# Performance work log

Hardware: AMD Instinct MI355X
Metric: run time of the kernel (lower is better)

The kernel has to match this reference:

```python
import jax, jax.numpy as jnp
import numpy as np


def setup_inputs() -> dict:
    key = jax.random.key(0)
    k1, k2, k3, k4, k5 = jax.random.split(key, 5)
    B, T, C = 64, 1024, 768
    scale = 1.0 / np.sqrt(C)
    tokens = jax.random.normal(k1, (B, T, C), dtype=jnp.float32)
    mask_topk = jax.random.randint(k2, (B, T), 0, 2) > 0
    Wq = jax.random.normal(k3, (C, C), dtype=jnp.float32) * scale
    Wk = jax.random.normal(k4, (C, C), dtype=jnp.float32) * scale
    Wv = jax.random.normal(k5, (C, C), dtype=jnp.float32) * scale
    return {"tokens": tokens, "mask_topk": mask_topk, "Wq": Wq, "Wk": Wk, "Wv": Wv}


def reference(tokens, mask_topk, Wq, Wk, Wv):
    # tokens: [B, T, C]; mask_topk: [B, T] bool; W*: [C, C] (torch Linear weight, y = x @ W.T)
    C = tokens.shape[-1]
    m = mask_topk.astype(tokens.dtype)                      # [B, T]
    cnt = jnp.sum(m, axis=-1, keepdims=True)                # [B, 1]
    masked_sum = jnp.einsum('btc,bt->bc', tokens, m)        # [B, C]
    mean_all = jnp.mean(tokens, axis=1)                     # fallback when mask is empty
    q_sal = jnp.where(cnt > 0, masked_sum / jnp.maximum(cnt, 1.0), mean_all)  # [B, C]
    q_sal = q_sal[:, None, :]                               # [B, 1, C]

    Q = jnp.einsum('bqc,dc->bqd', q_sal, Wq)                # [B, 1, C]
    K = jnp.einsum('btc,dc->btd', tokens, Wk)               # [B, T, C]
    V = jnp.einsum('btc,dc->btd', tokens, Wv)               # [B, T, C]

    scores = jnp.einsum('bqd,btd->bqt', Q, K) / jnp.sqrt(jnp.asarray(C, tokens.dtype))
    attn = jax.nn.softmax(scores, axis=-1)                  # [B, 1, T]
    v_fg = jnp.einsum('bqt,btd->bqd', attn, V)[:, 0, :]     # [B, C]
    return (v_fg, attn)
```

## Files before the change

kernel.cpp:

```cpp
#include <hip/hip_runtime.h>
#include <hip/hip_bf16.h>

#define B 64
#define T 1024
#define C 768
#define TSPLIT 32
#define TCHUNK (T / TSPLIT)

#define OFF_MSUM   64
#define OFF_ASUM   (OFF_MSUM + B*TSPLIT*C)
#define OFF_CNT    (OFF_ASUM + B*TSPLIT*C)
#define OFF_Q      (OFF_CNT + B*TSPLIT)
#define OFF_QK     (OFF_Q + B*C)
#define OFF_SCORES (OFF_QK + B*C)
#define OFF_MPART  (OFF_SCORES + B*T)
#define OFF_SPART  (OFF_MPART + B*TSPLIT)
#define OFF_PPART  (OFF_SPART + B*TSPLIT)

__device__ __forceinline__ bool read_mask(const void* mask, int mode, int idx) {
    if (mode == 1) return ((const unsigned char*)mask)[idx] != 0;
    if (mode == 2) return ((const float*)mask)[idx] != 0.0f;
    return ((const int*)mask)[idx] != 0;
}

__global__ void k_detect(const void* mask, int* mode_out) {
    __shared__ int s_not01, s_isf;
    int tid = threadIdx.x;
    if (tid == 0) { s_not01 = 0; s_isf = 0; }
    __syncthreads();
    const int* mi = (const int*)mask;
    int not01 = 0, isf = 0;
    for (int k = 0; k < 64; ++k) {
        int v = mi[tid + 256 * k];
        if (v != 0 && v != 1) not01 = 1;
        if (v == 0x3F800000) isf = 1;
    }
    if (not01) atomicOr(&s_not01, 1);
    if (isf)   atomicOr(&s_isf, 1);
    __syncthreads();
    if (tid == 0) *mode_out = s_isf ? 2 : (s_not01 ? 1 : 0);
}

__global__ __launch_bounds__(192) void
k_pass1(const float* __restrict__ tokens, const void* mask, const int* modep,
        float* __restrict__ msum, float* __restrict__ asum, float* __restrict__ cntpart) {
    int ts = blockIdx.x, b = blockIdx.y, tid = threadIdx.x;
    int mode = *modep;
    __shared__ float s_m[TCHUNK];
    if (tid < TCHUNK)
        s_m[tid] = read_mask(mask, mode, b * T + ts * TCHUNK + tid) ? 1.f : 0.f;
    __syncthreads();
    int c = tid * 4;
    float4 ms = {0, 0, 0, 0}, as = {0, 0, 0, 0};
    const float* tb = tokens + (size_t)b * T * C;
#pragma unroll 4
    for (int r = 0; r < TCHUNK; ++r) {
        int t = ts * TCHUNK + r;
        float4 x = *(const float4*)(tb + (size_t)t * C + c);
        as.x += x.x; as.y += x.y; as.z += x.z; as.w += x.w;
        float wm = s_m[r];
        ms.x += wm * x.x; ms.y += wm * x.y; ms.z += wm * x.z; ms.w += wm * x.w;
    }
    size_t o = (size_t)(b * TSPLIT + ts) * C + c;
    *(float4*)(msum + o) = ms;
    *(float4*)(asum + o) = as;
    if (tid == 0) {
        float cnt = 0.f;
#pragma unroll
        for (int r = 0; r < TCHUNK; ++r) cnt += s_m[r];
        cntpart[b * TSPLIT + ts] = cnt;
    }
}

__global__ __launch_bounds__(256) void
k_qsal_rowdot(const float* __restrict__ msum, const float* __restrict__ asum,
              const float* __restrict__ cntpart, const float* __restrict__ Wq,
              float* __restrict__ Qv) {
    int b = blockIdx.y, tid = threadIdx.x;
    __shared__ float sq[C];
    float cnt = 0.f;
#pragma unroll
    for (int p = 0; p < TSPLIT; ++p) cnt += cntpart[b * TSPLIT + p];
    bool um = (cnt > 0.f);
    float scale = um ? (1.f / fmaxf(cnt, 1.f)) : (1.f / (float)T);
    const float* src = um ? msum : asum;
    for (int c = tid; c < C; c += 256) {
        float a = 0.f;
#pragma unroll 8
        for (int p = 0; p < TSPLIT; ++p) a += src[(size_t)(b * TSPLIT + p) * C + c];
        sq[c] = a * scale;
    }
    __syncthreads();
    int d = blockIdx.x * 64 + (tid >> 2), sub = tid & 3;
    const float4* w = (const float4*)(Wq + (size_t)d * C);
    const float4* v4 = (const float4*)sq;
    float acc = 0.f;
#pragma unroll 8
    for (int j = sub * 48; j < sub * 48 + 48; ++j) {
        float4 a = v4[j], x = w[j];
        acc += a.x * x.x + a.y * x.y + a.z * x.z + a.w * x.w;
    }
    acc += __shfl_xor(acc, 1);
    acc += __shfl_xor(acc, 2);
    if (sub == 0) Qv[b * C + d] = acc;
}

__global__ __launch_bounds__(256) void
k_coldot(const float* __restrict__ Qv, const float* __restrict__ Wk,
         float* __restrict__ qk) {
    int b = blockIdx.y, tid = threadIdx.x;
    __shared__ float sQ[C];
    for (int c = tid; c < C; c += 256) sQ[c] = Qv[b * C + c];
    __syncthreads();
    int c = blockIdx.x * 64 + (tid >> 2), sub = tid & 3;
    float acc = 0.f;
#pragma unroll 8
    for (int i = 0; i < 192; ++i) {
        int d = sub * 192 + i;
        acc += sQ[d] * Wk[(size_t)d * C + c];
    }
    acc += __shfl_xor(acc, 1);
    acc += __shfl_xor(acc, 2);
    if (sub == 0) qk[b * C + c] = acc * 0.03608439182435161f;
}

__global__ __launch_bounds__(192) void
k_fused(const float* __restrict__ tokens, const float* __restrict__ qk,
        float* __restrict__ scores, float* __restrict__ mpart,
        float* __restrict__ spart, float* __restrict__ ppart) {
    __shared__ float sq[C];
    __shared__ float ssc[TCHUNK];
    __shared__ float sw[TCHUNK];
    int ts = blockIdx.x, b = blockIdx.y, tid = threadIdx.x;
    ((float4*)sq)[tid] = ((const float4*)(qk + (size_t)b * C))[tid];
    __syncthreads();
    int wave = tid >> 6, lane = tid & 63;
    const float* tb = tokens + (size_t)b * T * C;
    const float4* q4 = (const float4*)sq;
    for (int r = wave; r < TCHUNK; r += 3) {
        int t = ts * TCHUNK + r;
        const float4* row = (const float4*)(tb + (size_t)t * C);
        float acc = 0.f;
#pragma unroll
        for (int j = 0; j < 3; ++j) {
            int idx = lane + 64 * j;
            float4 x = row[idx], q = q4[idx];
            acc += x.x * q.x + x.y * q.y + x.z * q.z + x.w * q.w;
        }
        for (int s = 32; s > 0; s >>= 1) acc += __shfl_xor(acc, s);
        if (lane == 0) { ssc[r] = acc; scores[(size_t)b * T + t] = acc; }
    }
    __syncthreads();
    float m = -3.4e38f;
#pragma unroll
    for (int r = 0; r < TCHUNK; ++r) m = fmaxf(m, ssc[r]);
    if (tid < TCHUNK) sw[tid] = expf(ssc[tid] - m);
    __syncthreads();
    float s = 0.f;
#pragma unroll
    for (int r = 0; r < TCHUNK; ++r) s += sw[r];
    int c = tid * 4;
    float4 acc = {0, 0, 0, 0};
#pragma unroll 4
    for (int r = 0; r < TCHUNK; ++r) {
        int t = ts * TCHUNK + r;
        float wv = sw[r];
        float4 x = *(const float4*)(tb + (size_t)t * C + c);
        acc.x += wv * x.x; acc.y += wv * x.y; acc.z += wv * x.z; acc.w += wv * x.w;
    }
    *(float4*)(ppart + (size_t)(b * TSPLIT + ts) * C + c) = acc;
    if (tid == 0) { mpart[b * TSPLIT + ts] = m; spart[b * TSPLIT + ts] = s; }
}

__global__ __launch_bounds__(256) void
k_attn(const float* __restrict__ scores, const float* __restrict__ mpart,
       const float* __restrict__ spart, float* __restrict__ attn) {
    int b = blockIdx.x, tid = threadIdx.x;
    float M = -3.4e38f;
#pragma unroll
    for (int p = 0; p < TSPLIT; ++p) M = fmaxf(M, mpart[b * TSPLIT + p]);
    float Z = 0.f;
#pragma unroll
    for (int p = 0; p < TSPLIT; ++p) Z += spart[b * TSPLIT + p] * expf(mpart[b * TSPLIT + p] - M);
    float invZ = 1.f / Z;
    float4 sc = ((const float4*)(scores + (size_t)b * T))[tid];
    float4 o;
    o.x = expf(sc.x - M) * invZ; o.y = expf(sc.y - M) * invZ;
    o.z = expf(sc.z - M) * invZ; o.w = expf(sc.w - M) * invZ;
    ((float4*)(attn + (size_t)b * T))[tid] = o;
}

__global__ __launch_bounds__(256) void
k_vfg(const float* __restrict__ ppart, const float* __restrict__ mpart,
      const float* __restrict__ spart, const float* __restrict__ Wv,
      float* __restrict__ vfg) {
    int b = blockIdx.y, tid = threadIdx.x;
    __shared__ float sp[C];
    float M = -3.4e38f;
#pragma unroll
    for (int p = 0; p < TSPLIT; ++p) M = fmaxf(M, mpart[b * TSPLIT + p]);
    float Z = 0.f;
#pragma unroll
    for (int p = 0; p < TSPLIT; ++p) Z += spart[b * TSPLIT + p] * expf(mpart[b * TSPLIT + p] - M);
    float invZ = 1.f / Z;
    float coef[TSPLIT];
#pragma unroll
    for (int p = 0; p < TSPLIT; ++p) coef[p] = expf(mpart[b * TSPLIT + p] - M) * invZ;
    for (int c = tid; c < C; c += 256) {
        float a = 0.f;
#pragma unroll 8
        for (int p = 0; p < TSPLIT; ++p)
            a += coef[p] * ppart[(size_t)(b * TSPLIT + p) * C + c];
        sp[c] = a;
    }
    __syncthreads();
    int d = blockIdx.x * 64 + (tid >> 2), sub = tid & 3;
    const float4* w = (const float4*)(Wv + (size_t)d * C);
    const float4* v4 = (const float4*)sp;
    float acc = 0.f;
#pragma unroll 8
    for (int j = sub * 48; j < sub * 48 + 48; ++j) {
        float4 a = v4[j], x = w[j];
        acc += a.x * x.x + a.y * x.y + a.z * x.z + a.w * x.w;
    }
    acc += __shfl_xor(acc, 1);
    acc += __shfl_xor(acc, 2);
    if (sub == 0) vfg[b * C + d] = acc;
}

extern "C" void kernel_launch(void* const* d_in, const int* in_sizes, int n_in,
                              void* d_out, int out_size, void* d_ws, size_t ws_size,
                              hipStream_t stream) {
    const float* tokens = (const float*)d_in[0];
    const void*  mask   = d_in[1];
    const float* Wq     = (const float*)d_in[2];
    const float* Wk     = (const float*)d_in[3];
    const float* Wv     = (const float*)d_in[4];

    float* ws      = (float*)d_ws;
    int*   mode    = (int*)d_ws;
    float* msum    = ws + OFF_MSUM;
    float* asum    = ws + OFF_ASUM;
    float* cntpart = ws + OFF_CNT;
    float* Qv      = ws + OFF_Q;
    float* qk      = ws + OFF_QK;
    float* scores  = ws + OFF_SCORES;
    float* mpart   = ws + OFF_MPART;
    float* spart   = ws + OFF_SPART;
    float* ppart   = ws + OFF_PPART;

    float* v_fg = (float*)d_out;
    float* attn = (float*)d_out + B * C;

    k_detect<<<1, 256, 0, stream>>>(mask, mode);
    k_pass1<<<dim3(TSPLIT, B), 192, 0, stream>>>(tokens, mask, mode, msum, asum, cntpart);
    k_qsal_rowdot<<<dim3(12, B), 256, 0, stream>>>(msum, asum, cntpart, Wq, Qv);
    k_coldot<<<dim3(12, B), 256, 0, stream>>>(Qv, Wk, qk);
    k_fused<<<dim3(TSPLIT, B), 192, 0, stream>>>(tokens, qk, scores, mpart, spart, ppart);
    k_attn<<<B, 256, 0, stream>>>(scores, mpart, spart, attn);
    k_vfg<<<dim3(12, B), 256, 0, stream>>>(ppart, mpart, spart, Wv, v_fg);
}
```

Baseline: 172.4 us.

## Batch four rows per block in weight matvecs to reuse weight loads

Splits the pooling/reduction steps out of the Wq and Wv matvec kernels into separate kernels, then makes each matvec block handle four batch rows at once so each weight element loaded is reused four times. The Wk column-dot kernel is batched the same way. The aim is to cut redundant weight traffic, since the whole 768x768 weight matrix was previously reread once per batch. The cost is an extra kernel launch, an extra round trip of the pooled vectors through global memory, and fewer blocks (192 instead of 768) for the matvecs.

```diff
diff --git a/kernel.cpp b/kernel.cpp
--- a/kernel.cpp
+++ b/kernel.cpp
@@ -10,12 +10,14 @@
 #define OFF_MSUM   64
 #define OFF_ASUM   (OFF_MSUM + B*TSPLIT*C)
 #define OFF_CNT    (OFF_ASUM + B*TSPLIT*C)
-#define OFF_Q      (OFF_CNT + B*TSPLIT)
+#define OFF_QSAL   (OFF_CNT + B*TSPLIT)
+#define OFF_Q      (OFF_QSAL + B*C)
 #define OFF_QK     (OFF_Q + B*C)
 #define OFF_SCORES (OFF_QK + B*C)
 #define OFF_MPART  (OFF_SCORES + B*T)
 #define OFF_SPART  (OFF_MPART + B*TSPLIT)
 #define OFF_PPART  (OFF_SPART + B*TSPLIT)
+#define OFF_POOLED (OFF_PPART + B*TSPLIT*C)
 
 __device__ __forceinline__ bool read_mask(const void* mask, int mode, int idx) {
     if (mode == 1) return ((const unsigned char*)mask)[idx] != 0;
@@ -73,55 +75,84 @@
 }
 
 __global__ __launch_bounds__(256) void
-k_qsal_rowdot(const float* __restrict__ msum, const float* __restrict__ asum,
-              const float* __restrict__ cntpart, const float* __restrict__ Wq,
-              float* __restrict__ Qv) {
-    int b = blockIdx.y, tid = threadIdx.x;
-    __shared__ float sq[C];
+k_qsal(const float* __restrict__ msum, const float* __restrict__ asum,
+       const float* __restrict__ cntpart, float* __restrict__ qsal) {
+    int b = blockIdx.x, seg = blockIdx.y, tid = threadIdx.x;
     float cnt = 0.f;
 #pragma unroll
     for (int p = 0; p < TSPLIT; ++p) cnt += cntpart[b * TSPLIT + p];
     bool um = (cnt > 0.f);
     float scale = um ? (1.f / fmaxf(cnt, 1.f)) : (1.f / (float)T);
     const float* src = um ? msum : asum;
-    for (int c = tid; c < C; c += 256) {
-        float a = 0.f;
-#pragma unroll 8
-        for (int p = 0; p < TSPLIT; ++p) a += src[(size_t)(b * TSPLIT + p) * C + c];
-        sq[c] = a * scale;
-    }
-    __syncthreads();
-    int d = blockIdx.x * 64 + (tid >> 2), sub = tid & 3;
-    const float4* w = (const float4*)(Wq + (size_t)d * C);
-    const float4* v4 = (const float4*)sq;
-    float acc = 0.f;
+    int c = seg * 256 + tid;
+    float a = 0.f;
+#pragma unroll 8
+    for (int p = 0; p < TSPLIT; ++p) a += src[(size_t)(b * TSPLIT + p) * C + c];
+    qsal[b * C + c] = a * scale;
+}
+
+__global__ __launch_bounds__(256) void
+k_rowdot(const float* __restrict__ vin, const float* __restrict__ W,
+         float* __restrict__ vout, float scale) {
+    int bx = blockIdx.x, bg = blockIdx.y, tid = threadIdx.x;
+    __shared__ float4 sv[4][C / 4];
+    for (int i = tid; i < 4 * (C / 4); i += 256) {
+        int g = i / (C / 4), j = i % (C / 4);
+        sv[g][j] = ((const float4*)(vin + (size_t)(bg * 4 + g) * C))[j];
+    }
+    __syncthreads();
+    int d = bx * 64 + (tid >> 2), sub = tid & 3;
+    const float4* w = (const float4*)(W + (size_t)d * C);
+    float a0 = 0.f, a1 = 0.f, a2 = 0.f, a3 = 0.f;
 #pragma unroll 8
     for (int j = sub * 48; j < sub * 48 + 48; ++j) {
-        float4 a = v4[j], x = w[j];
-        acc += a.x * x.x + a.y * x.y + a.z * x.z + a.w * x.w;
-    }
-    acc += __shfl_xor(acc, 1);
-    acc += __shfl_xor(acc, 2);
-    if (sub == 0) Qv[b * C + d] = acc;
+        float4 x = w[j];
+        float4 v0 = sv[0][j], v1 = sv[1][j], v2 = sv[2][j], v3 = sv[3][j];
+        a0 += x.x * v0.x + x.y * v0.y + x.z * v0.z + x.w * v0.w;
+        a1 += x.x * v1.x + x.y * v1.y + x.z * v1.z + x.w * v1.w;
+        a2 += x.x * v2.x + x.y * v2.y + x.z * v2.z + x.w * v2.w;
+        a3 += x.x * v3.x + x.y * v3.y + x.z * v3.z + x.w * v3.w;
+    }
+    a0 += __shfl_xor(a0, 1); a0 += __shfl_xor(a0, 2);
+    a1 += __shfl_xor(a1, 1); a1 += __shfl_xor(a1, 2);
+    a2 += __shfl_xor(a2, 1); a2 += __shfl_xor(a2, 2);
+    a3 += __shfl_xor(a3, 1); a3 += __shfl_xor(a3, 2);
+    if (sub == 0) {
+        vout[(size_t)(bg * 4 + 0) * C + d] = a0 * scale;
+        vout[(size_t)(bg * 4 + 1) * C + d] = a1 * scale;
+        vout[(size_t)(bg * 4 + 2) * C + d] = a2 * scale;
+        vout[(size_t)(bg * 4 + 3) * C + d] = a3 * scale;
+    }
 }
 
 __global__ __launch_bounds__(256) void
 k_coldot(const float* __restrict__ Qv, const float* __restrict__ Wk,
          float* __restrict__ qk) {
-    int b = blockIdx.y, tid = threadIdx.x;
-    __shared__ float sQ[C];
-    for (int c = tid; c < C; c += 256) sQ[c] = Qv[b * C + c];
-    __syncthreads();
-    int c = blockIdx.x * 64 + (tid >> 2), sub = tid & 3;
-    float acc = 0.f;
+    int bx = blockIdx.x, bg = blockIdx.y, tid = threadIdx.x;
+    __shared__ float sQ[4][C];
+    for (int i = tid; i < 4 * C; i += 256)
+        sQ[i / C][i % C] = Qv[(size_t)(bg * 4 + i / C) * C + i % C];
+    __syncthreads();
+    int c = bx * 64 + (tid >> 2), sub = tid & 3;
+    float a0 = 0.f, a1 = 0.f, a2 = 0.f, a3 = 0.f;
 #pragma unroll 8
     for (int i = 0; i < 192; ++i) {
         int d = sub * 192 + i;
-        acc += sQ[d] * Wk[(size_t)d * C + c];
-    }
-    acc += __shfl_xor(acc, 1);
-    acc += __shfl_xor(acc, 2);
-    if (sub == 0) qk[b * C + c] = acc * 0.03608439182435161f;
+        float w = Wk[(size_t)d * C + c];
+        a0 += sQ[0][d] * w; a1 += sQ[1][d] * w;
+        a2 += sQ[2][d] * w; a3 += sQ[3][d] * w;
+    }
+    a0 += __shfl_xor(a0, 1); a0 += __shfl_xor(a0, 2);
+    a1 += __shfl_xor(a1, 1); a1 += __shfl_xor(a1, 2);
+    a2 += __shfl_xor(a2, 1); a2 += __shfl_xor(a2, 2);
+    a3 += __shfl_xor(a3, 1); a3 += __shfl_xor(a3, 2);
+    const float rsc = 0.03608439182435161f;
+    if (sub == 0) {
+        qk[(size_t)(bg * 4 + 0) * C + c] = a0 * rsc;
+        qk[(size_t)(bg * 4 + 1) * C + c] = a1 * rsc;
+        qk[(size_t)(bg * 4 + 2) * C + c] = a2 * rsc;
+        qk[(size_t)(bg * 4 + 3) * C + c] = a3 * rsc;
+    }
 }
 
 __global__ __launch_bounds__(192) void
@@ -173,9 +204,10 @@
 }
 
 __global__ __launch_bounds__(256) void
-k_attn(const float* __restrict__ scores, const float* __restrict__ mpart,
-       const float* __restrict__ spart, float* __restrict__ attn) {
-    int b = blockIdx.x, tid = threadIdx.x;
+k_pool_attn(const float* __restrict__ ppart, const float* __restrict__ scores,
+            const float* __restrict__ mpart, const float* __restrict__ spart,
+            float* __restrict__ pooled, float* __restrict__ attn) {
+    int bx = blockIdx.x, b = blockIdx.y, tid = threadIdx.x;
     float M = -3.4e38f;
 #pragma unroll
     for (int p = 0; p < TSPLIT; ++p) M = fmaxf(M, mpart[b * TSPLIT + p]);
@@ -183,49 +215,20 @@
 #pragma unroll
     for (int p = 0; p < TSPLIT; ++p) Z += spart[b * TSPLIT + p] * expf(mpart[b * TSPLIT + p] - M);
     float invZ = 1.f / Z;
-    float4 sc = ((const float4*)(scores + (size_t)b * T))[tid];
-    float4 o;
-    o.x = expf(sc.x - M) * invZ; o.y = expf(sc.y - M) * invZ;
-    o.z = expf(sc.z - M) * invZ; o.w = expf(sc.w - M) * invZ;
-    ((float4*)(attn + (size_t)b * T))[tid] = o;
-}
-
-__global__ __launch_bounds__(256) void
-k_vfg(const float* __restrict__ ppart, const float* __restrict__ mpart,
-      const float* __restrict__ spart, const float* __restrict__ Wv,
-      float* __restrict__ vfg) {
-    int b = blockIdx.y, tid = threadIdx.x;
-    __shared__ float sp[C];
-    float M = -3.4e38f;
-#pragma unroll
-    for (int p = 0; p < TSPLIT; ++p) M = fmaxf(M, mpart[b * TSPLIT + p]);
-    float Z = 0.f;
-#pragma unroll
-    for (int p = 0; p < TSPLIT; ++p) Z += spart[b * TSPLIT + p] * expf(mpart[b * TSPLIT + p] - M);
-    float invZ = 1.f / Z;
-    float coef[TSPLIT];
-#pragma unroll
-    for (int p = 0; p < TSPLIT; ++p) coef[p] = expf(mpart[b * TSPLIT + p] - M) * invZ;
-    for (int c = tid; c < C; c += 256) {
+    if (bx < 3) {
+        int c = bx * 256 + tid;
         float a = 0.f;
 #pragma unroll 8
         for (int p = 0; p < TSPLIT; ++p)
-            a += coef[p] * ppart[(size_t)(b * TSPLIT + p) * C + c];
-        sp[c] = a;
-    }
-    __syncthreads();
-    int d = blockIdx.x * 64 + (tid >> 2), sub = tid & 3;
-    const float4* w = (const float4*)(Wv + (size_t)d * C);
-    const float4* v4 = (const float4*)sp;
-    float acc = 0.f;
-#pragma unroll 8
-    for (int j = sub * 48; j < sub * 48 + 48; ++j) {
-        float4 a = v4[j], x = w[j];
-        acc += a.x * x.x + a.y * x.y + a.z * x.z + a.w * x.w;
-    }
-    acc += __shfl_xor(acc, 1);
-    acc += __shfl_xor(acc, 2);
-    if (sub == 0) vfg[b * C + d] = acc;
+            a += expf(mpart[b * TSPLIT + p] - M) * invZ * ppart[(size_t)(b * TSPLIT + p) * C + c];
+        pooled[b * C + c] = a;
+    } else {
+        float4 sc = ((const float4*)(scores + (size_t)b * T))[tid];
+        float4 o;
+        o.x = expf(sc.x - M) * invZ; o.y = expf(sc.y - M) * invZ;
+        o.z = expf(sc.z - M) * invZ; o.w = expf(sc.w - M) * invZ;
+        ((float4*)(attn + (size_t)b * T))[tid] = o;
+    }
 }
 
 extern "C" void kernel_launch(void* const* d_in, const int* in_sizes, int n_in,
@@ -242,21 +245,24 @@
     float* msum    = ws + OFF_MSUM;
     float* asum    = ws + OFF_ASUM;
     float* cntpart = ws + OFF_CNT;
+    float* qsal    = ws + OFF_QSAL;
     float* Qv      = ws + OFF_Q;
     float* qk      = ws + OFF_QK;
     float* scores  = ws + OFF_SCORES;
     float* mpart   = ws + OFF_MPART;
     float* spart   = ws + OFF_SPART;
     float* ppart   = ws + OFF_PPART;
+    float* pooled  = ws + OFF_POOLED;
 
     float* v_fg = (float*)d_out;
     float* attn = (float*)d_out + B * C;
 
     k_detect<<<1, 256, 0, stream>>>(mask, mode);
     k_pass1<<<dim3(TSPLIT, B), 192, 0, stream>>>(tokens, mask, mode, msum, asum, cntpart);
-    k_qsal_rowdot<<<dim3(12, B), 256, 0, stream>>>(msum, asum, cntpart, Wq, Qv);
-    k_coldot<<<dim3(12, B), 256, 0, stream>>>(Qv, Wk, qk);
+    k_qsal<<<dim3(B, 3), 256, 0, stream>>>(msum, asum, cntpart, qsal);
+    k_rowdot<<<dim3(12, 16), 256, 0, stream>>>(qsal, Wq, Qv, 1.0f);
+    k_coldot<<<dim3(12, 16), 256, 0, stream>>>(Qv, Wk, qk);
     k_fused<<<dim3(TSPLIT, B), 192, 0, stream>>>(tokens, qk, scores, mpart, spart, ppart);
-    k_attn<<<B, 256, 0, stream>>>(scores, mpart, spart, attn);
-    k_vfg<<<dim3(12, B), 256, 0, stream>>>(ppart, mpart, spart, Wv, v_fg);
-}
+    k_pool_attn<<<dim3(4, B), 256, 0, stream>>>(ppart, scores, mpart, spart, pooled, attn);
+    k_rowdot<<<dim3(12, 16), 256, 0, stream>>>(pooled, Wv, v_fg, 1.0f);
+}
```

Measured after the change: 187.5 us. 8.8% more time.
